# Optimization experiments

Hardware: AMD Instinct MI355X
Metric: run time of the kernel (lower is better)

Reference implementation:

```python
import jax, jax.numpy as jnp
import numpy as np
from jax import lax

T, B, C, HW = 64, 32, 4, 84
HID, A, FEAT = 256, 12, 1152  # 6*6*32 after 4 stride-2 convs on 84x84


def _conv(x, w, b):
    # NCHW input, OIHW kernel, stride 2, padding 1 (matches nn.Conv2d(k=3,s=2,p=1))
    y = lax.conv_general_dilated(x, w, (2, 2), ((1, 1), (1, 1)),
                                 dimension_numbers=('NCHW', 'OIHW', 'NCHW'))
    return y + b[None, :, None, None]


def setup_inputs() -> dict:
    key = jax.random.key(0)
    ks = jax.random.split(key, 16)
    inputs = jax.random.normal(ks[0], (T, B, C, HW, HW), dtype=jnp.float32)
    rnn_in = jax.random.normal(ks[1], (B, HID), dtype=jnp.float32)
    mask = jnp.ones((T, B, 1), dtype=jnp.float32)
    actions = jax.random.randint(ks[2], (T * B,), 0, A)
    s = 0.05
    w1 = jax.random.normal(ks[3], (32, C, 3, 3), jnp.float32) * s
    w2 = jax.random.normal(ks[4], (32, 32, 3, 3), jnp.float32) * s
    w3 = jax.random.normal(ks[5], (32, 32, 3, 3), jnp.float32) * s
    w4 = jax.random.normal(ks[6], (32, 32, 3, 3), jnp.float32) * s
    b1 = jnp.zeros((32,), jnp.float32); b2 = jnp.zeros((32,), jnp.float32)
    b3 = jnp.zeros((32,), jnp.float32); b4 = jnp.zeros((32,), jnp.float32)
    W_ih = jax.random.normal(ks[7], (3 * HID, FEAT), jnp.float32) * 0.02
    W_hh = jax.random.normal(ks[8], (3 * HID, HID), jnp.float32) * 0.02
    b_ih = jnp.zeros((3 * HID,), jnp.float32)
    b_hh = jnp.zeros((3 * HID,), jnp.float32)
    Wc = jax.random.normal(ks[9], (1, HID), jnp.float32) * 0.06
    bc = jnp.zeros((1,), jnp.float32)
    Wa = jax.random.normal(ks[10], (A, HID), jnp.float32) * 0.01
    ba = jnp.zeros((A,), jnp.float32)
    return {"inputs": inputs, "rnn_in": rnn_in, "mask": mask, "actions": actions,
            "w1": w1, "b1": b1, "w2": w2, "b2": b2, "w3": w3, "b3": b3,
            "w4": w4, "b4": b4, "W_ih": W_ih, "W_hh": W_hh, "b_ih": b_ih,
            "b_hh": b_hh, "Wc": Wc, "bc": bc, "Wa": Wa, "ba": ba}


def reference(inputs, rnn_in, mask, actions, w1, b1, w2, b2, w3, b3, w4, b4,
              W_ih, W_hh, b_ih, b_hh, Wc, bc, Wa, ba):
    Tl, Bl = inputs.shape[0], inputs.shape[1]
    x = inputs.reshape(Tl * Bl, inputs.shape[2], inputs.shape[3], inputs.shape[4])
    for w, b in ((w1, b1), (w2, b2), (w3, b3), (w4, b4)):
        x = jax.nn.elu(_conv(x, w, b))
    x = x.reshape(Tl, Bl, -1)  # [T, B, FEAT]

    def step(h, xm):
        x_t, m_t = xm
        h = h * m_t  # masked hidden reset
        gi = x_t @ W_ih.T + b_ih
        gh = h @ W_hh.T + b_hh
        i_r, i_z, i_n = jnp.split(gi, 3, axis=-1)
        h_r, h_z, h_n = jnp.split(gh, 3, axis=-1)
        r = jax.nn.sigmoid(i_r + h_r)
        z = jax.nn.sigmoid(i_z + h_z)
        n = jnp.tanh(i_n + r * h_n)
        h_new = (1.0 - z) * n + z * h
        return h_new, h_new

    h_final, outs = lax.scan(step, rnn_in, (x, mask))
    out = outs.reshape(Tl * Bl, HID)

    v = (out @ Wc.T + bc)[:, 0]
    logits = out @ Wa.T + ba
    logp = jax.nn.log_softmax(logits, axis=-1)
    logp_a = jnp.take_along_axis(logp, actions[:, None], axis=1)[:, 0]
    ent = -jnp.sum(jnp.exp(logp) * logp, axis=-1)
    return (v, actions, logp_a, ent, h_final)
```

## Files before the change

### kernel.cpp

```cpp
#include <hip/hip_runtime.h>
#include <hip/hip_bf16.h>
#include <math.h>

#define TT 64
#define BB 32
#define HID 256
#define NA 12
#define FEAT 1152
#define NB 2048
#define G3 768

typedef __hip_bfloat16 bf16;
typedef __attribute__((ext_vector_type(8))) short short8;
typedef __attribute__((ext_vector_type(4))) float f32x4;

static __device__ __forceinline__ float bf2f(bf16 v) { return __bfloat162float(v); }
static __device__ __forceinline__ bf16 f2bf(float v) { return __float2bfloat16(v); }

#define MFMA(a, b, c) __builtin_amdgcn_mfma_f32_16x16x32_bf16((a), (b), (c), 0, 0, 0)

__global__ __launch_bounds__(256) void prep_kernel(
    const float* __restrict__ w1, const float* __restrict__ w2,
    const float* __restrict__ w3, const float* __restrict__ w4,
    const float* __restrict__ W_ih, const float* __restrict__ W_hh,
    const float* __restrict__ b_ih, const float* __restrict__ b_hh,
    bf16* __restrict__ wB1, bf16* __restrict__ wB2,
    bf16* __restrict__ wB3, bf16* __restrict__ wB4,
    bf16* __restrict__ wihF, bf16* __restrict__ whh16, float* __restrict__ biasg)
{
    int i = blockIdx.x * 256 + threadIdx.x;
    if (i < 2048) {
        int j = i & 7, l = (i >> 3) & 63, rest = i >> 9;
        int ch = rest & 1, nt = rest >> 1;
        int k = ch * 32 + 8 * (l >> 4) + j;
        int co = nt * 16 + (l & 15);
        wB1[i] = f2bf(k < 36 ? w1[co * 36 + (k & 3) * 9 + (k >> 2)] : 0.0f);
    }
    if (i < 9216) {
        int j = i & 7, l = (i >> 3) & 63, rest = i >> 9;
        int kk = rest % 9, nt = rest / 9;
        int ci = 8 * (l >> 4) + j, co = nt * 16 + (l & 15);
        wB2[i] = f2bf(w2[co * 288 + ci * 9 + kk]);
        wB3[i] = f2bf(w3[co * 288 + ci * 9 + kk]);
        wB4[i] = f2bf(w4[co * 288 + ci * 9 + kk]);
    }
    if (i < 884736) {
        int j = i & 7, l = (i >> 3) & 63, rest = i >> 9;
        int st = rest % 48, ch = rest / 48;
        int k = ch * 32 + 8 * (l >> 4) + j, n = st * 16 + (l & 15);
        wihF[i] = f2bf(W_ih[(size_t)n * FEAT + k]);
    }
    if (i < 196608) {
        whh16[i] = f2bf(W_hh[i]);
    }
    if (i < G3) biasg[i] = b_ih[i] + (i < 2 * HID ? b_hh[i] : 0.0f);
}

__global__ __launch_bounds__(256) void conv1_kernel(
    const float* __restrict__ in, int n0,
    const bf16* __restrict__ wB1g, const float* __restrict__ b1,
    bf16* __restrict__ x1)
{
    __shared__ bf16 ins[7 * 84 * 4];
    __shared__ bf16 A[64 * 72];
    __shared__ bf16 wBs[2048];
    int tid = threadIdx.x;
    int nl = blockIdx.x / 28, blk = blockIdx.x % 28;
    int n = n0 + nl;
    int p0 = blk * 64;
    int oy_lo = p0 / 42;
    int oy_hi = (p0 + 63) / 42; if (oy_hi > 41) oy_hi = 41;
    int y_lo = 2 * oy_lo - 1;
    int rows = 2 * oy_hi + 2 - y_lo;

    if (tid < 256) ((uint4*)wBs)[tid] = ((const uint4*)wB1g)[tid];
    const float* inb = in + (size_t)n * 4 * 7056;
    for (int i = tid; i < rows * 336; i += 256) {
        int r = i / 336, rem = i % 336, ci = rem / 84, x = rem % 84;
        int y = y_lo + r;
        float v = (y >= 0) ? inb[ci * 7056 + y * 84 + x] : 0.0f;
        ins[(r * 84 + x) * 4 + ci] = f2bf(v);
    }
    __syncthreads();
    for (int i = tid; i < 576; i += 256) {
        int m = i / 9, q = i % 9;
        uint2 z; z.x = 0u; z.y = 0u;
        *(uint2*)&A[m * 72 + 36 + q * 4] = z;
    }
    for (int i = tid; i < 576; i += 256) {
        int m = i / 9, kk = i % 9;
        int kh = kk / 3, kw = kk - kh * 3;
        int p = p0 + m;
        uint2 v; v.x = 0u; v.y = 0u;
        if (p < 1764) {
            int oy = p / 42, ox = p - oy * 42;
            int y = 2 * oy - 1 + kh, x = 2 * ox - 1 + kw;
            if ((unsigned)y < 84u && (unsigned)x < 84u)
                v = *(const uint2*)&ins[((y - y_lo) * 84 + x) * 4];
        }
        *(uint2*)&A[m * 72 + kk * 4] = v;
    }
    __syncthreads();
    int lane = tid & 63, g = tid >> 6, quad = lane >> 4, c16 = lane & 15;
    int ma = g * 16 + c16;
    short8 a0 = *(const short8*)&A[ma * 72 + quad * 8];
    short8 a1 = *(const short8*)&A[ma * 72 + 32 + quad * 8];
    #pragma unroll
    for (int nt = 0; nt < 2; nt++) {
        float bv = b1[nt * 16 + c16];
        f32x4 acc = {bv, bv, bv, bv};
        short8 b0 = *(const short8*)&wBs[((nt * 2 + 0) * 64 + lane) * 8];
        short8 bq = *(const short8*)&wBs[((nt * 2 + 1) * 64 + lane) * 8];
        acc = MFMA(a0, b0, acc);
        acc = MFMA(a1, bq, acc);
        #pragma unroll
        for (int r = 0; r < 4; r++) {
            int p = p0 + g * 16 + 4 * quad + r;
            if (p < 1764) {
                float v = acc[r];
                v = v > 0.0f ? v : expm1f(v);
                x1[((size_t)nl * 1764 + p) * 32 + nt * 16 + c16] = f2bf(v);
            }
        }
    }
}

template<int HI, int HO, int OUTMODE>
__global__ __launch_bounds__(256) void convN_kernel(
    const bf16* __restrict__ xin, bf16* __restrict__ xout,
    const bf16* __restrict__ wBg, const float* __restrict__ bias, int n0)
{
    constexpr int NPIX = HO * HO;
    constexpr int NBLK = (NPIX + 63) / 64;
    __shared__ bf16 A[64 * 296];
    __shared__ bf16 wBs[9216];
    int tid = threadIdx.x;
    int nl = blockIdx.x / NBLK, blk = blockIdx.x % NBLK;
    int p0 = blk * 64;
    for (int i = tid; i < 1152; i += 256) ((uint4*)wBs)[i] = ((const uint4*)wBg)[i];
    const bf16* xb = xin + (size_t)nl * HI * HI * 32;
    for (int i = tid; i < 2304; i += 256) {
        int m = i / 36, t = i % 36, kk = t >> 2, part = t & 3;
        int kh = kk / 3, kw = kk - kh * 3;
        int p = p0 + m;
        uint4 v; v.x = v.y = v.z = v.w = 0u;
        if (p < NPIX) {
            int oy = p / HO, ox = p - oy * HO;
            int y = 2 * oy - 1 + kh, x = 2 * ox - 1 + kw;
            if ((unsigned)y < (unsigned)HI && (unsigned)x < (unsigned)HI)
                v = *(const uint4*)&xb[((size_t)(y * HI + x)) * 32 + part * 8];
        }
        *(uint4*)&A[m * 296 + kk * 32 + part * 8] = v;
    }
    __syncthreads();
    int lane = tid & 63, g = tid >> 6, quad = lane >> 4, c16 = lane & 15;
    int ma = g * 16 + c16;
    short8 af[9];
    #pragma unroll
    for (int kk = 0; kk < 9; kk++)
        af[kk] = *(const short8*)&A[ma * 296 + kk * 32 + quad * 8];
    #pragma unroll
    for (int nt = 0; nt < 2; nt++) {
        float bv = bias[nt * 16 + c16];
        f32x4 acc = {bv, bv, bv, bv};
        #pragma unroll
        for (int kk = 0; kk < 9; kk++) {
            short8 bfr = *(const short8*)&wBs[((nt * 9 + kk) * 64 + lane) * 8];
            acc = MFMA(af[kk], bfr, acc);
        }
        #pragma unroll
        for (int r = 0; r < 4; r++) {
            int p = p0 + g * 16 + 4 * quad + r;
            if (p < NPIX) {
                float v = acc[r];
                v = v > 0.0f ? v : expm1f(v);
                if (OUTMODE == 0)
                    xout[(((size_t)(n0 + nl)) * NPIX + p) * 32 + nt * 16 + c16] = f2bf(v);
                else
                    xout[(size_t)(n0 + nl) * FEAT + (nt * 16 + c16) * 36 + p] = f2bf(v);
            }
        }
    }
}

__global__ __launch_bounds__(256) void gemm_gi_kernel(
    const bf16* __restrict__ X, const bf16* __restrict__ wihF,
    const float* __restrict__ biasg, float* __restrict__ GI)
{
    __shared__ bf16 As[64 * 40];
    int tid = threadIdx.x;
    int m0 = blockIdx.x * 64, nb = blockIdx.y * 4, n0 = blockIdx.y * 64;
    int lane = tid & 63, g = tid >> 6, quad = lane >> 4, c16 = lane & 15;
    f32x4 acc[4];
    #pragma unroll
    for (int st = 0; st < 4; st++) {
        float bv = biasg[n0 + st * 16 + c16];
        acc[st] = (f32x4){bv, bv, bv, bv};
    }
    int sm = tid >> 2, sp = tid & 3;
    for (int ch = 0; ch < 36; ch++) {
        __syncthreads();
        *(uint4*)&As[sm * 40 + sp * 8] =
            *(const uint4*)&X[(size_t)(m0 + sm) * FEAT + ch * 32 + sp * 8];
        __syncthreads();
        short8 af = *(const short8*)&As[(g * 16 + c16) * 40 + quad * 8];
        #pragma unroll
        for (int st = 0; st < 4; st++) {
            short8 bfr = *(const short8*)&wihF[(((size_t)ch * 48 + nb + st) * 64 + lane) * 8];
            acc[st] = MFMA(af, bfr, acc[st]);
        }
    }
    #pragma unroll
    for (int st = 0; st < 4; st++)
        #pragma unroll
        for (int r = 0; r < 4; r++)
            GI[(size_t)(m0 + g * 16 + 4 * quad + r) * G3 + n0 + st * 16 + c16] = acc[st][r];
}

#define WDECL(i) uint4 w##i = wrow[i];
#define WDOT(i)  { uint4 w = w##i;                                             \
    float4 h0 = *(const float4*)&hs[(i) * 8];                                  \
    float4 h1 = *(const float4*)&hs[(i) * 8 + 4];                              \
    acc = fmaf(h0.x, __uint_as_float(w.x << 16), acc);                         \
    acc = fmaf(h0.y, __uint_as_float(w.x & 0xffff0000u), acc);                 \
    acc = fmaf(h0.z, __uint_as_float(w.y << 16), acc);                         \
    acc = fmaf(h0.w, __uint_as_float(w.y & 0xffff0000u), acc);                 \
    acc = fmaf(h1.x, __uint_as_float(w.z << 16), acc);                         \
    acc = fmaf(h1.y, __uint_as_float(w.z & 0xffff0000u), acc);                 \
    acc = fmaf(h1.z, __uint_as_float(w.w << 16), acc);                         \
    acc = fmaf(h1.w, __uint_as_float(w.w & 0xffff0000u), acc); }

__global__ __launch_bounds__(768, 3) void scan_kernel(
    const float* __restrict__ GI, const bf16* __restrict__ whh16,
    const float* __restrict__ b_hh, const float* __restrict__ rnn_in,
    const float* __restrict__ mask, float* __restrict__ H)
{
    __shared__ float hs[HID];
    __shared__ float pr[HID];
    __shared__ float pz[HID];
    __shared__ float pn[HID];
    int b = blockIdx.x, t = threadIdx.x;
    int gate = t >> 8, j = t & 255;

    const uint4* wrow = (const uint4*)(whh16 + (size_t)t * HID);
    WDECL(0)  WDECL(1)  WDECL(2)  WDECL(3)  WDECL(4)  WDECL(5)  WDECL(6)  WDECL(7)
    WDECL(8)  WDECL(9)  WDECL(10) WDECL(11) WDECL(12) WDECL(13) WDECL(14) WDECL(15)
    WDECL(16) WDECL(17) WDECL(18) WDECL(19) WDECL(20) WDECL(21) WDECL(22) WDECL(23)
    WDECL(24) WDECL(25) WDECL(26) WDECL(27) WDECL(28) WDECL(29) WDECL(30) WDECL(31)

    float bhn = (gate == 2) ? b_hh[2 * HID + j] : 0.0f;
    if (t < HID) hs[t] = rnn_in[b * HID + t] * mask[b];
    __syncthreads();

    for (int step = 0; step < TT; step++) {
        int row = step * BB + b;
        float gr = 0.f, gz = 0.f, gn = 0.f, hold = 0.f, mnext = 1.0f;
        if (gate == 0) {
            const float* gp = GI + (size_t)row * G3 + j;
            gr = gp[0]; gz = gp[256]; gn = gp[512];
            hold = hs[j];
            if (step + 1 < TT) mnext = mask[(step + 1) * BB + b];
        }
        float acc = bhn;
        WDOT(0)  WDOT(1)  WDOT(2)  WDOT(3)  WDOT(4)  WDOT(5)  WDOT(6)  WDOT(7)
        WDOT(8)  WDOT(9)  WDOT(10) WDOT(11) WDOT(12) WDOT(13) WDOT(14) WDOT(15)
        WDOT(16) WDOT(17) WDOT(18) WDOT(19) WDOT(20) WDOT(21) WDOT(22) WDOT(23)
        WDOT(24) WDOT(25) WDOT(26) WDOT(27) WDOT(28) WDOT(29) WDOT(30) WDOT(31)
        if (gate == 0)      pr[j] = acc;
        else if (gate == 1) pz[j] = acc;
        else                pn[j] = acc;
        __syncthreads();
        if (gate == 0) {
            float r = 1.0f / (1.0f + expf(-(gr + pr[j])));
            float z = 1.0f / (1.0f + expf(-(gz + pz[j])));
            float pre = gn + r * pn[j];
            pre = fminf(15.0f, fmaxf(-15.0f, pre));
            float e = expf(2.0f * pre);
            float nn = (e - 1.0f) / (e + 1.0f);
            float hnew = (1.0f - z) * nn + z * hold;
            H[(size_t)row * HID + j] = hnew;
            hs[j] = hnew * mnext;
        }
        __syncthreads();
    }
}

__global__ __launch_bounds__(256) void heads_kernel(
    const float* __restrict__ H, const int* __restrict__ actions,
    const float* __restrict__ Wc, const float* __restrict__ bc,
    const float* __restrict__ Wa, const float* __restrict__ ba,
    float* __restrict__ out)
{
    int r = blockIdx.x * 256 + threadIdx.x;
    if (r >= NB) return;
    const float* h = H + (size_t)r * HID;
    float v = bc[0];
    for (int k = 0; k < HID; k++) v += h[k] * Wc[k];
    float lg[NA];
    for (int a = 0; a < NA; a++) {
        float s = ba[a];
        const float* wa = Wa + a * HID;
        for (int k = 0; k < HID; k++) s += h[k] * wa[k];
        lg[a] = s;
    }
    float mx = lg[0];
    for (int a = 1; a < NA; a++) mx = fmaxf(mx, lg[a]);
    float Z = 0.f;
    for (int a = 0; a < NA; a++) Z += expf(lg[a] - mx);
    float lse = mx + logf(Z);
    int act = actions[r];
    float logp_a = lg[act] - lse;
    float ent = 0.f;
    for (int a = 0; a < NA; a++) {
        float lp = lg[a] - lse;
        ent -= expf(lp) * lp;
    }
    out[r]          = v;
    out[NB + r]     = (float)act;
    out[2 * NB + r] = logp_a;
    out[3 * NB + r] = ent;
}

__global__ __launch_bounds__(256) void hfin_kernel(const float* __restrict__ H, float* __restrict__ out)
{
    int i = blockIdx.x * 256 + threadIdx.x;
    if (i < BB * HID)
        out[4 * NB + i] = H[(size_t)(TT - 1) * BB * HID + i];
}

extern "C" void kernel_launch(void* const* d_in, const int* in_sizes, int n_in,
                              void* d_out, int out_size, void* d_ws, size_t ws_size,
                              hipStream_t stream) {
    const float* inputs  = (const float*)d_in[0];
    const float* rnn_in  = (const float*)d_in[1];
    const float* mask    = (const float*)d_in[2];
    const int*   actions = (const int*)d_in[3];
    const float* w1 = (const float*)d_in[4];
    const float* b1 = (const float*)d_in[5];
    const float* w2 = (const float*)d_in[6];
    const float* b2 = (const float*)d_in[7];
    const float* w3 = (const float*)d_in[8];
    const float* b3 = (const float*)d_in[9];
    const float* w4 = (const float*)d_in[10];
    const float* b4 = (const float*)d_in[11];
    const float* W_ih = (const float*)d_in[12];
    const float* W_hh = (const float*)d_in[13];
    const float* b_ih = (const float*)d_in[14];
    const float* b_hh = (const float*)d_in[15];
    const float* Wc = (const float*)d_in[16];
    const float* bc = (const float*)d_in[17];
    const float* Wa = (const float*)d_in[18];
    const float* ba = (const float*)d_in[19];
    float* out = (float*)d_out;

    char* ws = (char*)d_ws;
    size_t o = 0;
    auto nxt = [&](size_t b) { void* p = ws + o; o += (b + 255) & ~(size_t)255; return p; };
    bf16* wB1  = (bf16*)nxt(2048 * 2);
    bf16* wB2  = (bf16*)nxt(9216 * 2);
    bf16* wB3  = (bf16*)nxt(9216 * 2);
    bf16* wB4  = (bf16*)nxt(9216 * 2);
    bf16* wihF = (bf16*)nxt(884736 * 2);
    bf16* whh16 = (bf16*)nxt(196608 * 2);
    float* biasg = (float*)nxt(768 * 4);
    bf16* x4 = (bf16*)nxt((size_t)NB * FEAT * 2);
    bf16* x2 = (bf16*)nxt((size_t)NB * 441 * 32 * 2);

    const size_t X1_PER_IMG = 1764 * 32 * 2;
    const size_t TAILFIX = 15859712 + 6291456 + 2097152 + 1024;
    bf16* x3; float* GI; float* H; bf16* x1c;
    int CH;
    if (ws_size >= o + TAILFIX + 2048 * X1_PER_IMG + (1u << 20)) {
        CH = 2048;
        x3 = (bf16*)nxt(15859712); GI = (float*)nxt(6291456); H = (float*)nxt(2097152);
        x1c = (bf16*)nxt(2048 * X1_PER_IMG);
    } else if (ws_size >= o + TAILFIX + 512 * X1_PER_IMG + (1u << 20)) {
        CH = 512;
        x3 = (bf16*)nxt(15859712); GI = (float*)nxt(6291456); H = (float*)nxt(2097152);
        x1c = (bf16*)nxt(512 * X1_PER_IMG);
    } else if (ws_size >= o + TAILFIX + 256 * X1_PER_IMG + (1u << 20)) {
        CH = 256;
        x3 = (bf16*)nxt(15859712); GI = (float*)nxt(6291456); H = (float*)nxt(2097152);
        x1c = (bf16*)nxt(256 * X1_PER_IMG);
    } else {
        CH = 256;
        char* R1 = (char*)nxt(28901376);
        x1c = (bf16*)R1;
        x3  = (bf16*)R1;
        GI  = (float*)(R1 + 15859712);
        H   = (float*)(R1 + 15859712 + 6291456);
    }

    prep_kernel<<<3456, 256, 0, stream>>>(w1, w2, w3, w4, W_ih, W_hh, b_ih, b_hh,
                                          wB1, wB2, wB3, wB4, wihF, whh16, biasg);
    for (int c = 0; c < 2048 / CH; c++) {
        conv1_kernel<<<CH * 28, 256, 0, stream>>>(inputs, c * CH, wB1, b1, x1c);
        convN_kernel<42, 21, 0><<<CH * 7, 256, 0, stream>>>(x1c, x2, wB2, b2, c * CH);
    }
    convN_kernel<21, 11, 0><<<2048 * 2, 256, 0, stream>>>(x2, x3, wB3, b3, 0);
    convN_kernel<11, 6, 1><<<2048, 256, 0, stream>>>(x3, x4, wB4, b4, 0);
    gemm_gi_kernel<<<dim3(32, 12), 256, 0, stream>>>(x4, wihF, biasg, GI);
    scan_kernel<<<BB, 768, 0, stream>>>(GI, whh16, b_hh, rnn_in, mask, H);
    heads_kernel<<<NB / 256, 256, 0, stream>>>(H, actions, Wc, bc, Wa, ba, out);
    hfin_kernel<<<(BB * HID + 255) / 256, 256, 0, stream>>>(H, out);
}
```

Before: 1.645 ms.

## Fuse GRU gates per thread in scan kernel with double-buffered hidden state

Restructures the recurrent scan so each of 256 threads computes all three gate dot products for one hidden unit, instead of 768 threads each handling one gate row. This removes the shared gate-partial arrays and one barrier per step, and double-buffers the hidden state in shared memory so only a single sync per step remains. The trade-off is that recurrent weights are no longer held in registers and are streamed from memory/cache each step, with fewer waves per block.

```diff
diff --git a/kernel.cpp b/kernel.cpp
--- a/kernel.cpp
+++ b/kernel.cpp
@@ -13,6 +13,7 @@
 typedef __hip_bfloat16 bf16;
 typedef __attribute__((ext_vector_type(8))) short short8;
 typedef __attribute__((ext_vector_type(4))) float f32x4;
+typedef __attribute__((ext_vector_type(4))) unsigned int u32x4;
 
 static __device__ __forceinline__ float bf2f(bf16 v) { return __bfloat162float(v); }
 static __device__ __forceinline__ bf16 f2bf(float v) { return __float2bfloat16(v); }
@@ -217,70 +218,66 @@
             GI[(size_t)(m0 + g * 16 + 4 * quad + r) * G3 + n0 + st * 16 + c16] = acc[st][r];
 }
 
-#define WDECL(i) uint4 w##i = wrow[i];
-#define WDOT(i)  { uint4 w = w##i;                                             \
-    float4 h0 = *(const float4*)&hs[(i) * 8];                                  \
-    float4 h1 = *(const float4*)&hs[(i) * 8 + 4];                              \
-    acc = fmaf(h0.x, __uint_as_float(w.x << 16), acc);                         \
-    acc = fmaf(h0.y, __uint_as_float(w.x & 0xffff0000u), acc);                 \
-    acc = fmaf(h0.z, __uint_as_float(w.y << 16), acc);                         \
-    acc = fmaf(h0.w, __uint_as_float(w.y & 0xffff0000u), acc);                 \
-    acc = fmaf(h1.x, __uint_as_float(w.z << 16), acc);                         \
-    acc = fmaf(h1.y, __uint_as_float(w.z & 0xffff0000u), acc);                 \
-    acc = fmaf(h1.z, __uint_as_float(w.w << 16), acc);                         \
-    acc = fmaf(h1.w, __uint_as_float(w.w & 0xffff0000u), acc); }
-
-__global__ __launch_bounds__(768, 3) void scan_kernel(
+#define UNPK_LO(u) __uint_as_float((u) << 16)
+#define UNPK_HI(u) __uint_as_float((u) & 0xffff0000u)
+#define CF(W_, hb, A_) {                                                       \
+    float4 h0 = *(const float4*)&hcur[(hb)];                                   \
+    float4 h1 = *(const float4*)&hcur[(hb) + 4];                               \
+    A_ = fmaf(h0.x, UNPK_LO((W_).x), A_);                                      \
+    A_ = fmaf(h0.y, UNPK_HI((W_).x), A_);                                      \
+    A_ = fmaf(h0.z, UNPK_LO((W_).y), A_);                                      \
+    A_ = fmaf(h0.w, UNPK_HI((W_).y), A_);                                      \
+    A_ = fmaf(h1.x, UNPK_LO((W_).z), A_);                                      \
+    A_ = fmaf(h1.y, UNPK_HI((W_).z), A_);                                      \
+    A_ = fmaf(h1.z, UNPK_LO((W_).w), A_);                                      \
+    A_ = fmaf(h1.w, UNPK_HI((W_).w), A_); }
+
+__global__ __launch_bounds__(256)
+__attribute__((amdgpu_waves_per_eu(1, 2)))
+void scan_kernel(
     const float* __restrict__ GI, const bf16* __restrict__ whh16,
     const float* __restrict__ b_hh, const float* __restrict__ rnn_in,
     const float* __restrict__ mask, float* __restrict__ H)
 {
-    __shared__ float hs[HID];
-    __shared__ float pr[HID];
-    __shared__ float pz[HID];
-    __shared__ float pn[HID];
-    int b = blockIdx.x, t = threadIdx.x;
-    int gate = t >> 8, j = t & 255;
-
-    const uint4* wrow = (const uint4*)(whh16 + (size_t)t * HID);
-    WDECL(0)  WDECL(1)  WDECL(2)  WDECL(3)  WDECL(4)  WDECL(5)  WDECL(6)  WDECL(7)
-    WDECL(8)  WDECL(9)  WDECL(10) WDECL(11) WDECL(12) WDECL(13) WDECL(14) WDECL(15)
-    WDECL(16) WDECL(17) WDECL(18) WDECL(19) WDECL(20) WDECL(21) WDECL(22) WDECL(23)
-    WDECL(24) WDECL(25) WDECL(26) WDECL(27) WDECL(28) WDECL(29) WDECL(30) WDECL(31)
-
-    float bhn = (gate == 2) ? b_hh[2 * HID + j] : 0.0f;
-    if (t < HID) hs[t] = rnn_in[b * HID + t] * mask[b];
+    __shared__ float hsd[2][HID];
+    int b = blockIdx.x, j = threadIdx.x;
+
+    const u32x4* pr0 = (const u32x4*)(whh16 + (size_t)j * HID);
+    const u32x4* pr1 = (const u32x4*)(whh16 + (size_t)(j + 256) * HID);
+    const u32x4* pr2 = (const u32x4*)(whh16 + (size_t)(j + 512) * HID);
+    float bhn = b_hh[2 * HID + j];
+
+    float hloc = rnn_in[b * HID + j] * mask[b];
+    hsd[0][j] = hloc;
     __syncthreads();
 
+    #pragma unroll 1
     for (int step = 0; step < TT; step++) {
         int row = step * BB + b;
-        float gr = 0.f, gz = 0.f, gn = 0.f, hold = 0.f, mnext = 1.0f;
-        if (gate == 0) {
-            const float* gp = GI + (size_t)row * G3 + j;
-            gr = gp[0]; gz = gp[256]; gn = gp[512];
-            hold = hs[j];
-            if (step + 1 < TT) mnext = mask[(step + 1) * BB + b];
-        }
-        float acc = bhn;
-        WDOT(0)  WDOT(1)  WDOT(2)  WDOT(3)  WDOT(4)  WDOT(5)  WDOT(6)  WDOT(7)
-        WDOT(8)  WDOT(9)  WDOT(10) WDOT(11) WDOT(12) WDOT(13) WDOT(14) WDOT(15)
-        WDOT(16) WDOT(17) WDOT(18) WDOT(19) WDOT(20) WDOT(21) WDOT(22) WDOT(23)
-        WDOT(24) WDOT(25) WDOT(26) WDOT(27) WDOT(28) WDOT(29) WDOT(30) WDOT(31)
-        if (gate == 0)      pr[j] = acc;
-        else if (gate == 1) pz[j] = acc;
-        else                pn[j] = acc;
-        __syncthreads();
-        if (gate == 0) {
-            float r = 1.0f / (1.0f + expf(-(gr + pr[j])));
-            float z = 1.0f / (1.0f + expf(-(gz + pz[j])));
-            float pre = gn + r * pn[j];
-            pre = fminf(15.0f, fmaxf(-15.0f, pre));
-            float e = expf(2.0f * pre);
-            float nn = (e - 1.0f) / (e + 1.0f);
-            float hnew = (1.0f - z) * nn + z * hold;
-            H[(size_t)row * HID + j] = hnew;
-            hs[j] = hnew * mnext;
-        }
+        const float* gp = GI + (size_t)row * G3 + j;
+        float gr = gp[0], gz = gp[256], gn = gp[512];
+        float mnext = (step + 1 < TT) ? mask[(step + 1) * BB + b] : 1.0f;
+
+        const float* hcur = hsd[step & 1];
+        float ar = 0.f, az = 0.f, an = bhn;
+        #pragma unroll
+        for (int c = 0; c < 32; c++) {
+            u32x4 w0 = pr0[c], w1 = pr1[c], w2 = pr2[c];
+            CF(w0, c * 8, ar)
+            CF(w1, c * 8, az)
+            CF(w2, c * 8, an)
+        }
+
+        float r_ = 1.0f / (1.0f + expf(-(gr + ar)));
+        float z_ = 1.0f / (1.0f + expf(-(gz + az)));
+        float pre = gn + r_ * an;
+        pre = fminf(15.0f, fmaxf(-15.0f, pre));
+        float e = expf(2.0f * pre);
+        float nn = (e - 1.0f) / (e + 1.0f);
+        float hnew = (1.0f - z_) * nn + z_ * hloc;
+        H[(size_t)row * HID + j] = hnew;
+        hloc = hnew * mnext;
+        hsd[(step + 1) & 1][j] = hloc;
         __syncthreads();
     }
 }
@@ -400,7 +397,7 @@
     convN_kernel<21, 11, 0><<<2048 * 2, 256, 0, stream>>>(x2, x3, wB3, b3, 0);
     convN_kernel<11, 6, 1><<<2048, 256, 0, stream>>>(x3, x4, wB4, b4, 0);
     gemm_gi_kernel<<<dim3(32, 12), 256, 0, stream>>>(x4, wihF, biasg, GI);
-    scan_kernel<<<BB, 768, 0, stream>>>(GI, whh16, b_hh, rnn_in, mask, H);
+    scan_kernel<<<BB, 256, 0, stream>>>(GI, whh16, b_hh, rnn_in, mask, H);
     heads_kernel<<<NB / 256, 256, 0, stream>>>(H, actions, Wc, bc, Wa, ba, out);
     hfin_kernel<<<(BB * HID + 255) / 256, 256, 0, stream>>>(H, out);
 }
```

Result: slower. 2.692 ms (+63.7%).
